# Kernel optimization log

Hardware: AMD Instinct MI355X
Metric: run time of the kernel (lower is better)

Reference implementation:

```python
import jax, jax.numpy as jnp
import numpy as np

B, Q, K, H = 8, 2048, 2048, 512


def setup_inputs() -> dict:
    key = jax.random.key(0)
    ks = jax.random.split(key, 12)
    s = 1.0 / np.sqrt(H)
    return {
        "query": jax.random.normal(ks[0], (B, Q, H), jnp.float32),
        "key_": jax.random.normal(ks[1], (B, K, H), jnp.float32),
        "value": jax.random.normal(ks[2], (B, K, H), jnp.float32),
        "mask": jax.random.randint(ks[3], (B, K), 0, 2).astype(bool),
        "Wq": jax.random.normal(ks[4], (H, H), jnp.float32) * s,
        "bq": jnp.zeros((H,), jnp.float32),
        "Wk": jax.random.normal(ks[5], (H, H), jnp.float32) * s,
        "bk": jnp.zeros((H,), jnp.float32),
        "Wv": jax.random.normal(ks[6], (H, H), jnp.float32) * s,
        "bv": jnp.zeros((H,), jnp.float32),
        "Wo": jax.random.normal(ks[7], (H, H), jnp.float32) * s,
        "bo": jnp.zeros((H,), jnp.float32),
    }


def reference(query, key_, value, mask, Wq, bq, Wk, bk, Wv, bv, Wo, bo):
    scale = jnp.sqrt(jnp.float32(H))
    Qp = query @ Wq + bq          # (B,Q,H)
    Kp = key_ @ Wk + bk           # (B,K,H)
    Vp = value @ Wv + bv          # (B,K,H)
    energy = jnp.einsum("bqh,bkh->bqk", Qp, Kp) / scale
    # mask is (B, key_len); torch code broadcasts it over all query rows
    energy = jnp.where(mask[:, None, :], -jnp.inf, energy)
    idx = jnp.argmax(energy, axis=-1)                 # (B,Q)
    score = jax.nn.one_hot(idx, K, dtype=energy.dtype)  # hardmax one-hot (B,Q,K)
    # score @ V is exactly a per-row gather of the argmax-selected V row
    res = jnp.take_along_axis(Vp, idx[:, :, None], axis=1)  # (B,Q,H)
    res = res @ Wo + bo
    return (res, score)
```

## Files before the change

kernel.cpp:

```cpp
#include <hip/hip_runtime.h>

typedef _Float16 f16;
typedef f16 f16x8 __attribute__((ext_vector_type(8)));
typedef f16 f16x4 __attribute__((ext_vector_type(4)));
typedef short s16x8 __attribute__((ext_vector_type(8)));
typedef short s16x4 __attribute__((ext_vector_type(4)));
typedef float f32x4 __attribute__((ext_vector_type(4)));

#define MFMA16(a,b,c)  __builtin_amdgcn_mfma_f32_16x16x32_f16(a,b,c,0,0,0)
#define MFMAB16(a,b,c) __builtin_amdgcn_mfma_f32_16x16x32_bf16(a,b,c,0,0,0)

static constexpr int Bn = 8, Qn = 2048, Kn = 2048, Hn = 512;
static constexpr int Mn = Bn * Qn;

typedef __attribute__((address_space(1))) const unsigned int as1_uint;
typedef __attribute__((address_space(3))) unsigned int as3_uint;

__device__ __forceinline__ void gl_lds16(const void* g, void* l) {
    __builtin_amdgcn_global_load_lds((as1_uint*)g, (as3_uint*)l, 16, 0, 0);
}

__device__ __forceinline__ short bf16r(float x) {
    unsigned u = __builtin_bit_cast(unsigned, x);
    u += 0x7fffu + ((u >> 16) & 1u);
    return (short)(u >> 16);
}

__device__ __forceinline__ int swz(int row) { return (row >> 1) & 3; }

__global__ __launch_bounds__(256) void compact_mask(
    const int* __restrict__ mask, int* __restrict__ cidx, int* __restrict__ cnt)
{
    __shared__ int sums[256];
    int b = blockIdx.x, t = threadIdx.x;
    int base = b * Kn + t * 8;
    int mv[8]; int s = 0;
    #pragma unroll
    for (int i = 0; i < 8; ++i) { mv[i] = (mask[base + i] == 0); s += mv[i]; }
    sums[t] = s;
    __syncthreads();
    for (int off = 1; off < 256; off <<= 1) {
        int v = (t >= off) ? sums[t - off] : 0;
        __syncthreads();
        sums[t] += v;
        __syncthreads();
    }
    int pos = (t > 0 ? sums[t - 1] : 0);
    #pragma unroll
    for (int i = 0; i < 8; ++i)
        if (mv[i]) cidx[b * Kn + pos++] = t * 8 + i;
    if (t == 255) {
        int total = sums[255];
        if (total == 0) { cidx[b * Kn] = 0; total = 1; }
        cnt[b] = total;
    }
}

__global__ __launch_bounds__(256) void prep_w(
    const float* __restrict__ Wq, const float* __restrict__ Wk,
    const float* __restrict__ Wv, const float* __restrict__ Wo,
    f16* __restrict__ Wqth, f16* __restrict__ Wqtl,
    f16* __restrict__ Wkth, f16* __restrict__ Wktl,
    short* __restrict__ Wvt, short* __restrict__ Wot)
{
    int e = blockIdx.x * 256 + threadIdx.x;
    int k = e >> 9, n = e & 511;
    int s = k * 512 + n, d = n * 512 + k;
    float wq = Wq[s] * 512.0f;
    f16 h = (f16)wq;
    Wqth[d] = h; Wqtl[d] = (f16)((wq - (float)h) * 2048.0f);
    float wk = Wk[s] * 512.0f;
    h = (f16)wk;
    Wkth[d] = h; Wktl[d] = (f16)((wk - (float)h) * 2048.0f);
    Wvt[d] = bf16r(Wv[s]);
    Wot[d] = bf16r(Wo[s]);
}

__global__ __launch_bounds__(256) void proj_fused(
    const float* __restrict__ query, const float* __restrict__ key_,
    const float* __restrict__ value,
    const f16* __restrict__ Wqth, const f16* __restrict__ Wqtl,
    const f16* __restrict__ Wkth, const f16* __restrict__ Wktl,
    const short* __restrict__ Wvt,
    const float* __restrict__ bq, const float* __restrict__ bk,
    const float* __restrict__ bvec,
    f16* __restrict__ Qp_h, f16* __restrict__ Qp_l,
    f16* __restrict__ Kc_h, f16* __restrict__ Kc_l,
    short* __restrict__ Vc,
    const int* __restrict__ cidx, const int* __restrict__ cnt)
{
    __shared__ __align__(16) char smem[49152];
    const int which = blockIdx.z;
    const int tid = threadIdx.x, lane = tid & 63, wid = tid >> 6;
    const int l15 = lane & 15, lg = lane >> 4;
    const int m0 = blockIdx.x * 64, n0 = blockIdx.y * 128;
    const int b = m0 >> 11, m0l = m0 & 2047;
    const int srow = lane >> 2, sg = lane & 3;
    const int ar0 = tid >> 3, ac0 = (tid & 7) * 4;

    int cn = 0;
    if (which > 0) {
        cn = cnt[b];
        if (m0l >= cn) return;
    }
    const float* Aptr = (which == 0) ? query : (which == 1 ? key_ : value);
    const float* aSrc[2];
    #pragma unroll
    for (int rr = 0; rr < 2; ++rr) {
        int row = ar0 + rr * 32;
        size_t grow;
        if (which > 0) {
            int r = m0l + row;
            int cid = (r < cn) ? cidx[b * Kn + r] : 0;
            grow = (size_t)(b * Kn + cid);
        } else {
            grow = (size_t)(m0 + row);
        }
        aSrc[rr] = Aptr + grow * Hn;
    }

    if (which < 2) {
        f16 (*Ah)[2048] = (f16(*)[2048])(smem);
        f16 (*Al)[2048] = (f16(*)[2048])(smem + 8192);
        f16 (*Bh)[4096] = (f16(*)[4096])(smem + 16384);
        f16 (*Bl)[4096] = (f16(*)[4096])(smem + 32768);
        const f16* Bth = (which == 0) ? Wqth : Wkth;
        const f16* Btl = (which == 0) ? Wqtl : Wktl;
        const float* bias = (which == 0) ? bq : bk;
        f16* Ph = (which == 0) ? Qp_h : Kc_h;
        f16* Pl = (which == 0) ? Qp_l : Kc_l;

        auto stageB = [&](int buf, int ks) {
            const int k0 = ks << 5;
            #pragma unroll
            for (int h = 0; h < 2; ++h) {
                int s = wid + h * 4;
                int row = s * 16 + srow;
                int goff = k0 + ((sg ^ swz(row)) << 3);
                gl_lds16(Bth + (size_t)(n0 + row) * Hn + goff, &Bh[buf][s * 512]);
                gl_lds16(Btl + (size_t)(n0 + row) * Hn + goff, &Bl[buf][s * 512]);
            }
        };
        auto writeA = [&](int buf, const f32x4* av) {
            #pragma unroll
            for (int rr = 0; rr < 2; ++rr) {
                int row = ar0 + rr * 32;
                f16x4 oh, ol;
                #pragma unroll
                for (int j = 0; j < 4; ++j) {
                    f16 hh = (f16)av[rr][j];
                    oh[j] = hh;
                    ol[j] = (f16)((av[rr][j] - (float)hh) * 2048.0f);
                }
                int off = row * 32 + (((ac0 >> 3) ^ swz(row)) << 3) + (ac0 & 7);
                *(f16x4*)&Ah[buf][off] = oh;
                *(f16x4*)&Al[buf][off] = ol;
            }
        };

        f32x4 a0[4][2] = {}, a1[4][2] = {};
        {
            f32x4 av[2];
            #pragma unroll
            for (int rr = 0; rr < 2; ++rr) av[rr] = *(const f32x4*)(aSrc[rr] + ac0);
            stageB(0, 0);
            writeA(0, av);
        }
        __syncthreads();
        #pragma unroll 1
        for (int ks = 0; ks < 16; ++ks) {
            const int cur = ks & 1, nxt = cur ^ 1;
            f32x4 av[2];
            if (ks < 15) {
                const int k1 = (ks + 1) << 5;
                #pragma unroll
                for (int rr = 0; rr < 2; ++rr) av[rr] = *(const f32x4*)(aSrc[rr] + k1 + ac0);
                stageB(nxt, ks + 1);
            }
            f16x8 fbh[2], fbl[2];
            #pragma unroll
            for (int fj = 0; fj < 2; ++fj) {
                int row = wid * 32 + fj * 16 + l15;
                int off = row * 32 + ((lg ^ swz(row)) << 3);
                fbh[fj] = *(f16x8*)&Bh[cur][off];
                fbl[fj] = *(f16x8*)&Bl[cur][off];
            }
            #pragma unroll
            for (int fi = 0; fi < 4; ++fi) {
                int row = fi * 16 + l15;
                int off = row * 32 + ((lg ^ swz(row)) << 3);
                f16x8 fah = *(f16x8*)&Ah[cur][off];
                f16x8 fal = *(f16x8*)&Al[cur][off];
                #pragma unroll
                for (int fj = 0; fj < 2; ++fj) {
                    a0[fi][fj] = MFMA16(fah, fbh[fj], a0[fi][fj]);
                    a1[fi][fj] = MFMA16(fah, fbl[fj], a1[fi][fj]);
                    a1[fi][fj] = MFMA16(fal, fbh[fj], a1[fi][fj]);
                }
            }
            if (ks < 15) writeA(nxt, av);
            __syncthreads();
        }
        #pragma unroll
        for (int fi = 0; fi < 4; ++fi)
        #pragma unroll
        for (int fj = 0; fj < 2; ++fj)
        #pragma unroll
        for (int j = 0; j < 4; ++j) {
            int m = m0 + fi * 16 + lg * 4 + j;
            int n = n0 + wid * 32 + fj * 16 + l15;
            float v = (a0[fi][fj][j] + a1[fi][fj][j] * (1.0f / 2048.0f)) * (1.0f / 512.0f) + bias[n];
            f16 h = (f16)v;
            Ph[(size_t)m * Hn + n] = h;
            Pl[(size_t)m * Hn + n] = (f16)((v - (float)h) * 2048.0f);
        }
    } else {
        short (*As)[2048] = (short(*)[2048])(smem);
        short (*Bs)[4096] = (short(*)[4096])(smem + 8192);

        auto stageB = [&](int buf, int ks) {
            const int k0 = ks << 5;
            #pragma unroll
            for (int h = 0; h < 2; ++h) {
                int s = wid + h * 4;
                int row = s * 16 + srow;
                int goff = k0 + ((sg ^ swz(row)) << 3);
                gl_lds16(Wvt + (size_t)(n0 + row) * Hn + goff, &Bs[buf][s * 512]);
            }
        };
        auto writeA = [&](int buf, const f32x4* av) {
            #pragma unroll
            for (int rr = 0; rr < 2; ++rr) {
                int row = ar0 + rr * 32;
                s16x4 o;
                #pragma unroll
                for (int j = 0; j < 4; ++j) o[j] = bf16r(av[rr][j]);
                int off = row * 32 + (((ac0 >> 3) ^ swz(row)) << 3) + (ac0 & 7);
                *(s16x4*)&As[buf][off] = o;
            }
        };

        f32x4 acc[4][2] = {};
        {
            f32x4 av[2];
            #pragma unroll
            for (int rr = 0; rr < 2; ++rr) av[rr] = *(const f32x4*)(aSrc[rr] + ac0);
            stageB(0, 0);
            writeA(0, av);
        }
        __syncthreads();
        #pragma unroll 1
        for (int ks = 0; ks < 16; ++ks) {
            const int cur = ks & 1, nxt = cur ^ 1;
            f32x4 av[2];
            if (ks < 15) {
                const int k1 = (ks + 1) << 5;
                #pragma unroll
                for (int rr = 0; rr < 2; ++rr) av[rr] = *(const f32x4*)(aSrc[rr] + k1 + ac0);
                stageB(nxt, ks + 1);
            }
            s16x8 fb[2];
            #pragma unroll
            for (int fj = 0; fj < 2; ++fj) {
                int row = wid * 32 + fj * 16 + l15;
                fb[fj] = *(s16x8*)&Bs[cur][row * 32 + ((lg ^ swz(row)) << 3)];
            }
            #pragma unroll
            for (int fi = 0; fi < 4; ++fi) {
                int row = fi * 16 + l15;
                s16x8 fa = *(s16x8*)&As[cur][row * 32 + ((lg ^ swz(row)) << 3)];
                #pragma unroll
                for (int fj = 0; fj < 2; ++fj)
                    acc[fi][fj] = MFMAB16(fa, fb[fj], acc[fi][fj]);
            }
            if (ks < 15) writeA(nxt, av);
            __syncthreads();
        }
        #pragma unroll
        for (int fi = 0; fi < 4; ++fi)
        #pragma unroll
        for (int fj = 0; fj < 2; ++fj)
        #pragma unroll
        for (int j = 0; j < 4; ++j) {
            int m = m0 + fi * 16 + lg * 4 + j;
            int n = n0 + wid * 32 + fj * 16 + l15;
            Vc[(size_t)m * Hn + n] = bf16r(acc[fi][fj][j] + bvec[n]);
        }
    }
}

__global__ __launch_bounds__(256) void energy_argmax(
    const f16* __restrict__ Qh, const f16* __restrict__ Ql,
    const f16* __restrict__ Kh, const f16* __restrict__ Kl,
    const int* __restrict__ cnt,
    float* __restrict__ pval, int* __restrict__ pidx)
{
    __shared__ __align__(16) f16 Ah[2][2048], Al[2][2048], Bh[2][4096], Bl[2][4096];
    __shared__ float bwv[4][64];
    __shared__ int   bwi[4][64];
    const int tid = threadIdx.x, lane = tid & 63, wid = tid >> 6;
    const int l15 = lane & 15, lg = lane >> 4;
    const int qt = blockIdx.x, kc = blockIdx.y, b = blockIdx.z;
    const int cn = cnt[b];
    const int kbase = kc << 7;
    if (kbase >= cn) return;
    const int m0 = b * Qn + qt * 64;
    const int kr0 = b * Kn + kbase;
    const float NEGINF = -__builtin_inff();
    const int srow = lane >> 2, sg = lane & 3;

    auto stage = [&](int buf, int ks) {
        const int k0 = ks << 5;
        {
            int row = wid * 16 + srow;
            int goff = k0 + ((sg ^ swz(row)) << 3);
            size_t ga = (size_t)(m0 + row) * Hn + goff;
            gl_lds16(Qh + ga, &Ah[buf][wid * 512]);
            gl_lds16(Ql + ga, &Al[buf][wid * 512]);
        }
        #pragma unroll
        for (int h = 0; h < 2; ++h) {
            int s = wid + h * 4;
            int row = s * 16 + srow;
            int goff = k0 + ((sg ^ swz(row)) << 3);
            size_t gb = (size_t)(kr0 + row) * Hn + goff;
            gl_lds16(Kh + gb, &Bh[buf][s * 512]);
            gl_lds16(Kl + gb, &Bl[buf][s * 512]);
        }
    };

    f32x4 a0[4][2] = {}, a1[4][2] = {};
    stage(0, 0);
    __syncthreads();
    #pragma unroll 1
    for (int ks = 0; ks < 16; ++ks) {
        const int cur = ks & 1;
        if (ks < 15) stage(cur ^ 1, ks + 1);
        f16x8 fbh[2], fbl[2];
        #pragma unroll
        for (int fj = 0; fj < 2; ++fj) {
            int row = wid * 32 + fj * 16 + l15;
            int off = row * 32 + ((lg ^ swz(row)) << 3);
            fbh[fj] = *(f16x8*)&Bh[cur][off];
            fbl[fj] = *(f16x8*)&Bl[cur][off];
        }
        #pragma unroll
        for (int fi = 0; fi < 4; ++fi) {
            int row = fi * 16 + l15;
            int off = row * 32 + ((lg ^ swz(row)) << 3);
            f16x8 fah = *(f16x8*)&Ah[cur][off];
            f16x8 fal = *(f16x8*)&Al[cur][off];
            #pragma unroll
            for (int fj = 0; fj < 2; ++fj) {
                a0[fi][fj] = MFMA16(fah, fbh[fj], a0[fi][fj]);
                a1[fi][fj] = MFMA16(fah, fbl[fj], a1[fi][fj]);
                a1[fi][fj] = MFMA16(fal, fbh[fj], a1[fi][fj]);
            }
        }
        __syncthreads();
    }
    #pragma unroll
    for (int fi = 0; fi < 4; ++fi) {
        #pragma unroll
        for (int j = 0; j < 4; ++j) {
            float bv = NEGINF; int bc = 0x7fffffff;
            #pragma unroll
            for (int fj = 0; fj < 2; ++fj) {
                int lc = wid * 32 + fj * 16 + l15;
                float v = a0[fi][fj][j] + a1[fi][fj][j] * (1.0f / 2048.0f);
                v = (kbase + lc < cn) ? v : NEGINF;
                if (v > bv || (v == bv && lc < bc)) { bv = v; bc = lc; }
            }
            #pragma unroll
            for (int sm = 1; sm < 16; sm <<= 1) {
                float ov = __shfl_xor(bv, sm, 64);
                int   oc = __shfl_xor(bc, sm, 64);
                if (ov > bv || (ov == bv && oc < bc)) { bv = ov; bc = oc; }
            }
            if (l15 == 0) {
                int row = fi * 16 + lg * 4 + j;
                bwv[wid][row] = bv; bwi[wid][row] = bc;
            }
        }
    }
    __syncthreads();
    if (tid < 64) {
        float bv = bwv[0][tid]; int bc = bwi[0][tid];
        #pragma unroll
        for (int s = 1; s < 4; ++s) {
            float v = bwv[s][tid]; int i = bwi[s][tid];
            if (v > bv || (v == bv && i < bc)) { bv = v; bc = i; }
        }
        int m = m0 + tid;
        pval[m * 16 + kc] = bv;
        pidx[m * 16 + kc] = kbase + bc;
    }
}

__global__ __launch_bounds__(256) void merge_gather(
    const float* __restrict__ pval, const int* __restrict__ pidx,
    const int* __restrict__ cnt, const int* __restrict__ cidx,
    const short* __restrict__ Vc, short* __restrict__ Vg, int* __restrict__ idxArr)
{
    int wid = threadIdx.x >> 6, lane = threadIdx.x & 63;
    int m = blockIdx.x * 4 + wid;
    int b = m >> 11;
    int nc = (cnt[b] + 127) >> 7;
    float bv = -__builtin_inff(); int bi = 0x7fffffff;
    for (int c = 0; c < nc; ++c) {
        float v = pval[m * 16 + c]; int i = pidx[m * 16 + c];
        if (v > bv || (v == bv && i < bi)) { bv = v; bi = i; }
    }
    if (lane == 0) idxArr[m] = cidx[b * Kn + bi];
    size_t src = ((size_t)(b * Kn + bi)) * Hn + lane * 8;
    size_t dst = (size_t)m * Hn + lane * 8;
    *(s16x8*)(Vg + dst) = *(const s16x8*)(Vc + src);
}

__global__ __launch_bounds__(256) void gemm_o(
    const short* __restrict__ A, const short* __restrict__ Bt,
    const float* __restrict__ bias, float* __restrict__ Out)
{
    __shared__ __align__(16) short As[2][4096], Bs[2][4096];
    const int tid = threadIdx.x, lane = tid & 63, wid = tid >> 6;
    const int wr = wid >> 1, wc = wid & 1, l15 = lane & 15, lg = lane >> 4;
    const int m0 = blockIdx.x * 128, n0 = blockIdx.y * 128;
    const int srow = lane >> 2, sg = lane & 3;
    f32x4 acc[4][4] = {};

    auto stage = [&](int buf, int ks) {
        const int k0 = ks << 5;
        #pragma unroll
        for (int h = 0; h < 2; ++h) {
            int s = wid + h * 4;
            int row = s * 16 + srow;
            int goff = k0 + ((sg ^ swz(row)) << 3);
            gl_lds16(A  + (size_t)(m0 + row) * Hn + goff, &As[buf][s * 512]);
            gl_lds16(Bt + (size_t)(n0 + row) * Hn + goff, &Bs[buf][s * 512]);
        }
    };

    stage(0, 0);
    __syncthreads();
    #pragma unroll 1
    for (int ks = 0; ks < 16; ++ks) {
        const int cur = ks & 1;
        if (ks < 15) stage(cur ^ 1, ks + 1);
        s16x8 fb[4];
        #pragma unroll
        for (int fj = 0; fj < 4; ++fj) {
            int row = wc * 64 + fj * 16 + l15;
            fb[fj] = *(s16x8*)&Bs[cur][row * 32 + ((lg ^ swz(row)) << 3)];
        }
        #pragma unroll
        for (int fi = 0; fi < 4; ++fi) {
            int row = wr * 64 + fi * 16 + l15;
            s16x8 fa = *(s16x8*)&As[cur][row * 32 + ((lg ^ swz(row)) << 3)];
            #pragma unroll
            for (int fj = 0; fj < 4; ++fj)
                acc[fi][fj] = MFMAB16(fa, fb[fj], acc[fi][fj]);
        }
        __syncthreads();
    }
    #pragma unroll
    for (int fi = 0; fi < 4; ++fi)
    #pragma unroll
    for (int fj = 0; fj < 4; ++fj)
    #pragma unroll
    for (int j = 0; j < 4; ++j) {
        int m = m0 + wr * 64 + fi * 16 + lg * 4 + j;
        int n = n0 + wc * 64 + fj * 16 + l15;
        Out[(size_t)m * Hn + n] = acc[fi][fj][j] + bias[n];
    }
}

__global__ __launch_bounds__(256) void score_fill(
    const int* __restrict__ idxArr, float* __restrict__ score)
{
    int m = blockIdx.x;
    int c = idxArr[m];
    float* row = score + (size_t)m * Kn;
    int t = threadIdx.x;
    #pragma unroll
    for (int i = 0; i < 2; ++i) {
        int v = t + i * 256;
        f32x4 val = {0.f, 0.f, 0.f, 0.f};
        if ((c >> 2) == v) val[c & 3] = 1.0f;
        *(f32x4*)(row + v * 4) = val;
    }
}

extern "C" void kernel_launch(void* const* d_in, const int* in_sizes, int n_in,
                              void* d_out, int out_size, void* d_ws, size_t ws_size,
                              hipStream_t stream)
{
    const float* query = (const float*)d_in[0];
    const float* key_  = (const float*)d_in[1];
    const float* value = (const float*)d_in[2];
    const int*   mask  = (const int*)d_in[3];
    const float* Wq = (const float*)d_in[4];
    const float* bq = (const float*)d_in[5];
    const float* Wk = (const float*)d_in[6];
    const float* bk = (const float*)d_in[7];
    const float* Wv = (const float*)d_in[8];
    const float* bv = (const float*)d_in[9];
    const float* Wo = (const float*)d_in[10];
    const float* bo = (const float*)d_in[11];

    float* res = (float*)d_out;
    float* scoreBase = res + (size_t)Mn * Hn;
    char* sc = (char*)scoreBase;
    const size_t MB16 = (size_t)Mn * Hn * 2;
    f16*   Qp_h = (f16*)(sc + 0 * MB16);
    f16*   Qp_l = (f16*)(sc + 1 * MB16);
    f16*   Kc_h = (f16*)(sc + 2 * MB16);
    f16*   Kc_l = (f16*)(sc + 3 * MB16);
    short* Vc   = (short*)(sc + 4 * MB16);
    char*  wb   = sc + 5 * MB16;
    f16*   Wqth = (f16*)(wb + 0 * 524288);
    f16*   Wqtl = (f16*)(wb + 1 * 524288);
    f16*   Wkth = (f16*)(wb + 2 * 524288);
    f16*   Wktl = (f16*)(wb + 3 * 524288);
    short* Wvt  = (short*)(wb + 4 * 524288);
    short* Wot  = (short*)(wb + 5 * 524288);
    int*   cidx = (int*)(wb + 6 * 524288);
    float* pval = (float*)(wb + 6 * 524288 + 65536);
    int*   pidx = (int*)(wb + 6 * 524288 + 65536 + 1048576);
    short* Vg   = (short*)(sc + 0 * MB16);

    int*   idxArr = (int*)d_ws;
    int*   cnt    = (int*)d_ws + Mn;

    compact_mask<<<Bn, 256, 0, stream>>>(mask, cidx, cnt);
    prep_w<<<1024, 256, 0, stream>>>(Wq, Wk, Wv, Wo, Wqth, Wqtl, Wkth, Wktl, Wvt, Wot);

    proj_fused<<<dim3(Mn / 64, Hn / 128, 3), 256, 0, stream>>>(
        query, key_, value, Wqth, Wqtl, Wkth, Wktl, Wvt,
        bq, bk, bv, Qp_h, Qp_l, Kc_h, Kc_l, Vc, cidx, cnt);

    energy_argmax<<<dim3(Qn / 64, 16, Bn), 256, 0, stream>>>(
        Qp_h, Qp_l, Kc_h, Kc_l, cnt, pval, pidx);

    merge_gather<<<Mn / 4, 256, 0, stream>>>(pval, pidx, cnt, cidx, Vc, Vg, idxArr);

    gemm_o<<<dim3(Mn / 128, Hn / 128), 256, 0, stream>>>(Vg, Wot, bo, res);

    score_fill<<<Mn, 256, 0, stream>>>(idxArr, scoreBase);
}
```

Measured before the change: 239.0 us.

## Fold weight products algebraically to skip K/V projections and gather raw inputs

Rewrites the pipeline using associativity. Wq·Wkᵀ and Wv·Wo are precomputed as small weight products, so the query is projected once through the combined matrix and the energy uses raw keys plus a per-key bias term. The V projection and the separate output GEMM become one GEMM on the gathered raw value rows. The score one-hot is now written with a memset followed by a scatter of ones instead of a full fill kernel. This removes the per-key K and V projection GEMMs and the intermediate V buffers, but adds small prep GEMMs and changes rounding behaviour, since the products are formed before splitting to f16/bf16.

```diff
diff --git a/kernel.cpp b/kernel.cpp
--- a/kernel.cpp
+++ b/kernel.cpp
@@ -56,243 +56,281 @@
     }
 }
 
-__global__ __launch_bounds__(256) void prep_w(
-    const float* __restrict__ Wq, const float* __restrict__ Wk,
-    const float* __restrict__ Wv, const float* __restrict__ Wo,
-    f16* __restrict__ Wqth, f16* __restrict__ Wqtl,
-    f16* __restrict__ Wkth, f16* __restrict__ Wktl,
-    short* __restrict__ Wvt, short* __restrict__ Wot)
+__global__ __launch_bounds__(256) void prep_split(
+    const float* __restrict__ Wk, const float* __restrict__ Wo,
+    f16* __restrict__ Wk_h, f16* __restrict__ Wk_l, short* __restrict__ Wot)
 {
     int e = blockIdx.x * 256 + threadIdx.x;
-    int k = e >> 9, n = e & 511;
-    int s = k * 512 + n, d = n * 512 + k;
-    float wq = Wq[s] * 512.0f;
-    f16 h = (f16)wq;
-    Wqth[d] = h; Wqtl[d] = (f16)((wq - (float)h) * 2048.0f);
-    float wk = Wk[s] * 512.0f;
-    h = (f16)wk;
-    Wkth[d] = h; Wktl[d] = (f16)((wk - (float)h) * 2048.0f);
-    Wvt[d] = bf16r(Wv[s]);
-    Wot[d] = bf16r(Wo[s]);
-}
-
-__global__ __launch_bounds__(256) void proj_fused(
-    const float* __restrict__ query, const float* __restrict__ key_,
-    const float* __restrict__ value,
-    const f16* __restrict__ Wqth, const f16* __restrict__ Wqtl,
-    const f16* __restrict__ Wkth, const f16* __restrict__ Wktl,
-    const short* __restrict__ Wvt,
-    const float* __restrict__ bq, const float* __restrict__ bk,
-    const float* __restrict__ bvec,
-    f16* __restrict__ Qp_h, f16* __restrict__ Qp_l,
-    f16* __restrict__ Kc_h, f16* __restrict__ Kc_l,
-    short* __restrict__ Vc,
-    const int* __restrict__ cidx, const int* __restrict__ cnt)
-{
-    __shared__ __align__(16) char smem[49152];
-    const int which = blockIdx.z;
+    float v = Wk[e] * 512.0f;
+    f16 h = (f16)v;
+    Wk_h[e] = h; Wk_l[e] = (f16)((v - (float)h) * 2048.0f);
+    int r = e >> 9, c = e & 511;
+    Wot[c * 512 + r] = bf16r(Wo[e]);
+}
+
+__global__ __launch_bounds__(512) void prep_vec(
+    const float* __restrict__ Wk, const float* __restrict__ Wo,
+    const float* __restrict__ bq, const float* __restrict__ bv,
+    const float* __restrict__ bo,
+    float* __restrict__ wvec, float* __restrict__ cvec)
+{
+    int t = threadIdx.x;
+    float s = 0.f;
+    for (int n = 0; n < 512; n += 4) {
+        f32x4 a = *(const f32x4*)(Wk + (size_t)t * 512 + n);
+        f32x4 q = *(const f32x4*)(bq + n);
+        s += a[0]*q[0] + a[1]*q[1] + a[2]*q[2] + a[3]*q[3];
+    }
+    wvec[t] = s;
+    float s2 = 0.f;
+    for (int h = 0; h < 512; ++h) s2 += bv[h] * Wo[h * 512 + t];
+    cvec[t] = s2 + bo[t];
+}
+
+template<int PREP>
+__global__ __launch_bounds__(256) void gemm_split(
+    const float* __restrict__ Af,
+    const f16* __restrict__ Bh_g, const f16* __restrict__ Bl_g,
+    f16* __restrict__ Oh, f16* __restrict__ Ol)
+{
+    __shared__ __align__(16) f16 Ah[2][2048], Al[2][2048], Bh[2][4096], Bl[2][4096];
     const int tid = threadIdx.x, lane = tid & 63, wid = tid >> 6;
     const int l15 = lane & 15, lg = lane >> 4;
     const int m0 = blockIdx.x * 64, n0 = blockIdx.y * 128;
-    const int b = m0 >> 11, m0l = m0 & 2047;
     const int srow = lane >> 2, sg = lane & 3;
     const int ar0 = tid >> 3, ac0 = (tid & 7) * 4;
 
-    int cn = 0;
-    if (which > 0) {
-        cn = cnt[b];
-        if (m0l >= cn) return;
-    }
-    const float* Aptr = (which == 0) ? query : (which == 1 ? key_ : value);
+    auto stageB = [&](int buf, int ks) {
+        const int k0 = ks << 5;
+        #pragma unroll
+        for (int h = 0; h < 2; ++h) {
+            int s = wid + h * 4;
+            int row = s * 16 + srow;
+            int goff = k0 + ((sg ^ swz(row)) << 3);
+            gl_lds16(Bh_g + (size_t)(n0 + row) * Hn + goff, &Bh[buf][s * 512]);
+            gl_lds16(Bl_g + (size_t)(n0 + row) * Hn + goff, &Bl[buf][s * 512]);
+        }
+    };
+    auto writeA = [&](int buf, const f32x4* av) {
+        #pragma unroll
+        for (int rr = 0; rr < 2; ++rr) {
+            int row = ar0 + rr * 32;
+            f16x4 oh, ol;
+            #pragma unroll
+            for (int j = 0; j < 4; ++j) {
+                f16 hh = (f16)av[rr][j];
+                oh[j] = hh;
+                ol[j] = (f16)((av[rr][j] - (float)hh) * 2048.0f);
+            }
+            int off = row * 32 + (((ac0 >> 3) ^ swz(row)) << 3) + (ac0 & 7);
+            *(f16x4*)&Ah[buf][off] = oh;
+            *(f16x4*)&Al[buf][off] = ol;
+        }
+    };
+
+    const float* aSrc[2];
+    #pragma unroll
+    for (int rr = 0; rr < 2; ++rr)
+        aSrc[rr] = Af + (size_t)(m0 + ar0 + rr * 32) * Hn;
+
+    f32x4 a0[4][2] = {}, a1[4][2] = {};
+    {
+        f32x4 av[2];
+        #pragma unroll
+        for (int rr = 0; rr < 2; ++rr) av[rr] = *(const f32x4*)(aSrc[rr] + ac0);
+        stageB(0, 0);
+        writeA(0, av);
+    }
+    __syncthreads();
+    #pragma unroll 1
+    for (int ks = 0; ks < 16; ++ks) {
+        const int cur = ks & 1, nxt = cur ^ 1;
+        f32x4 av[2];
+        if (ks < 15) {
+            const int k1 = (ks + 1) << 5;
+            #pragma unroll
+            for (int rr = 0; rr < 2; ++rr) av[rr] = *(const f32x4*)(aSrc[rr] + k1 + ac0);
+            stageB(nxt, ks + 1);
+        }
+        f16x8 fbh[2], fbl[2];
+        #pragma unroll
+        for (int fj = 0; fj < 2; ++fj) {
+            int row = wid * 32 + fj * 16 + l15;
+            int off = row * 32 + ((lg ^ swz(row)) << 3);
+            fbh[fj] = *(f16x8*)&Bh[cur][off];
+            fbl[fj] = *(f16x8*)&Bl[cur][off];
+        }
+        #pragma unroll
+        for (int fi = 0; fi < 4; ++fi) {
+            int row = fi * 16 + l15;
+            int off = row * 32 + ((lg ^ swz(row)) << 3);
+            f16x8 fah = *(f16x8*)&Ah[cur][off];
+            f16x8 fal = *(f16x8*)&Al[cur][off];
+            #pragma unroll
+            for (int fj = 0; fj < 2; ++fj) {
+                a0[fi][fj] = MFMA16(fah, fbh[fj], a0[fi][fj]);
+                a1[fi][fj] = MFMA16(fah, fbl[fj], a1[fi][fj]);
+                a1[fi][fj] = MFMA16(fal, fbh[fj], a1[fi][fj]);
+            }
+        }
+        if (ks < 15) writeA(nxt, av);
+        __syncthreads();
+    }
+    #pragma unroll
+    for (int fi = 0; fi < 4; ++fi)
+    #pragma unroll
+    for (int fj = 0; fj < 2; ++fj)
+    #pragma unroll
+    for (int j = 0; j < 4; ++j) {
+        int m = m0 + fi * 16 + lg * 4 + j;
+        int n = n0 + wid * 32 + fj * 16 + l15;
+        float v = a0[fi][fj][j] + a1[fi][fj][j] * (1.0f / 2048.0f);
+        if (PREP == 0) v *= (1.0f / 512.0f);
+        f16 h = (f16)v;
+        f16 lo = (f16)((v - (float)h) * 2048.0f);
+        size_t o = PREP ? ((size_t)n * Hn + m) : ((size_t)m * Hn + n);
+        Oh[o] = h; Ol[o] = lo;
+    }
+}
+
+template<int MODE>
+__global__ __launch_bounds__(256) void gemm_bfk(
+    const float* __restrict__ Af, const short* __restrict__ Bt,
+    const float* __restrict__ cvec, const int* __restrict__ idxArr,
+    void* __restrict__ Out)
+{
+    __shared__ __align__(16) short As[2][2048], Bs[2][4096];
+    const int tid = threadIdx.x, lane = tid & 63, wid = tid >> 6;
+    const int l15 = lane & 15, lg = lane >> 4;
+    const int m0 = blockIdx.x * 64, n0 = blockIdx.y * 128;
+    const int srow = lane >> 2, sg = lane & 3;
+    const int ar0 = tid >> 3, ac0 = (tid & 7) * 4;
+
     const float* aSrc[2];
     #pragma unroll
     for (int rr = 0; rr < 2; ++rr) {
         int row = ar0 + rr * 32;
         size_t grow;
-        if (which > 0) {
-            int r = m0l + row;
-            int cid = (r < cn) ? cidx[b * Kn + r] : 0;
-            grow = (size_t)(b * Kn + cid);
+        if (MODE == 1) {
+            int b = m0 >> 11;
+            grow = (size_t)(b * Kn + idxArr[m0 + row]);
         } else {
             grow = (size_t)(m0 + row);
         }
-        aSrc[rr] = Aptr + grow * Hn;
-    }
-
-    if (which < 2) {
-        f16 (*Ah)[2048] = (f16(*)[2048])(smem);
-        f16 (*Al)[2048] = (f16(*)[2048])(smem + 8192);
-        f16 (*Bh)[4096] = (f16(*)[4096])(smem + 16384);
-        f16 (*Bl)[4096] = (f16(*)[4096])(smem + 32768);
-        const f16* Bth = (which == 0) ? Wqth : Wkth;
-        const f16* Btl = (which == 0) ? Wqtl : Wktl;
-        const float* bias = (which == 0) ? bq : bk;
-        f16* Ph = (which == 0) ? Qp_h : Kc_h;
-        f16* Pl = (which == 0) ? Qp_l : Kc_l;
-
-        auto stageB = [&](int buf, int ks) {
-            const int k0 = ks << 5;
-            #pragma unroll
-            for (int h = 0; h < 2; ++h) {
-                int s = wid + h * 4;
-                int row = s * 16 + srow;
-                int goff = k0 + ((sg ^ swz(row)) << 3);
-                gl_lds16(Bth + (size_t)(n0 + row) * Hn + goff, &Bh[buf][s * 512]);
-                gl_lds16(Btl + (size_t)(n0 + row) * Hn + goff, &Bl[buf][s * 512]);
-            }
-        };
-        auto writeA = [&](int buf, const f32x4* av) {
-            #pragma unroll
-            for (int rr = 0; rr < 2; ++rr) {
-                int row = ar0 + rr * 32;
-                f16x4 oh, ol;
-                #pragma unroll
-                for (int j = 0; j < 4; ++j) {
-                    f16 hh = (f16)av[rr][j];
-                    oh[j] = hh;
-                    ol[j] = (f16)((av[rr][j] - (float)hh) * 2048.0f);
-                }
-                int off = row * 32 + (((ac0 >> 3) ^ swz(row)) << 3) + (ac0 & 7);
-                *(f16x4*)&Ah[buf][off] = oh;
-                *(f16x4*)&Al[buf][off] = ol;
-            }
-        };
-
-        f32x4 a0[4][2] = {}, a1[4][2] = {};
-        {
-            f32x4 av[2];
-            #pragma unroll
-            for (int rr = 0; rr < 2; ++rr) av[rr] = *(const f32x4*)(aSrc[rr] + ac0);
-            stageB(0, 0);
-            writeA(0, av);
-        }
+        aSrc[rr] = Af + grow * Hn;
+    }
+
+    auto stageB = [&](int buf, int ks) {
+        const int k0 = ks << 5;
+        #pragma unroll
+        for (int h = 0; h < 2; ++h) {
+            int s = wid + h * 4;
+            int row = s * 16 + srow;
+            int goff = k0 + ((sg ^ swz(row)) << 3);
+            gl_lds16(Bt + (size_t)(n0 + row) * Hn + goff, &Bs[buf][s * 512]);
+        }
+    };
+    auto writeA = [&](int buf, const f32x4* av) {
+        #pragma unroll
+        for (int rr = 0; rr < 2; ++rr) {
+            int row = ar0 + rr * 32;
+            s16x4 o;
+            #pragma unroll
+            for (int j = 0; j < 4; ++j) o[j] = bf16r(av[rr][j]);
+            int off = row * 32 + (((ac0 >> 3) ^ swz(row)) << 3) + (ac0 & 7);
+            *(s16x4*)&As[buf][off] = o;
+        }
+    };
+
+    f32x4 acc[4][2] = {};
+    {
+        f32x4 av[2];
+        #pragma unroll
+        for (int rr = 0; rr < 2; ++rr) av[rr] = *(const f32x4*)(aSrc[rr] + ac0);
+        stageB(0, 0);
+        writeA(0, av);
+    }
+    __syncthreads();
+    #pragma unroll 1
+    for (int ks = 0; ks < 16; ++ks) {
+        const int cur = ks & 1, nxt = cur ^ 1;
+        f32x4 av[2];
+        if (ks < 15) {
+            const int k1 = (ks + 1) << 5;
+            #pragma unroll
+            for (int rr = 0; rr < 2; ++rr) av[rr] = *(const f32x4*)(aSrc[rr] + k1 + ac0);
+            stageB(nxt, ks + 1);
+        }
+        s16x8 fb[2];
+        #pragma unroll
+        for (int fj = 0; fj < 2; ++fj) {
+            int row = wid * 32 + fj * 16 + l15;
+            fb[fj] = *(s16x8*)&Bs[cur][row * 32 + ((lg ^ swz(row)) << 3)];
+        }
+        #pragma unroll
+        for (int fi = 0; fi < 4; ++fi) {
+            int row = fi * 16 + l15;
+            s16x8 fa = *(s16x8*)&As[cur][row * 32 + ((lg ^ swz(row)) << 3)];
+            #pragma unroll
+            for (int fj = 0; fj < 2; ++fj)
+                acc[fi][fj] = MFMAB16(fa, fb[fj], acc[fi][fj]);
+        }
+        if (ks < 15) writeA(nxt, av);
         __syncthreads();
-        #pragma unroll 1
-        for (int ks = 0; ks < 16; ++ks) {
-            const int cur = ks & 1, nxt = cur ^ 1;
-            f32x4 av[2];
-            if (ks < 15) {
-                const int k1 = (ks + 1) << 5;
-                #pragma unroll
-                for (int rr = 0; rr < 2; ++rr) av[rr] = *(const f32x4*)(aSrc[rr] + k1 + ac0);
-                stageB(nxt, ks + 1);
-            }
-            f16x8 fbh[2], fbl[2];
-            #pragma unroll
-            for (int fj = 0; fj < 2; ++fj) {
-                int row = wid * 32 + fj * 16 + l15;
-                int off = row * 32 + ((lg ^ swz(row)) << 3);
-                fbh[fj] = *(f16x8*)&Bh[cur][off];
-                fbl[fj] = *(f16x8*)&Bl[cur][off];
-            }
-            #pragma unroll
-            for (int fi = 0; fi < 4; ++fi) {
-                int row = fi * 16 + l15;
-                int off = row * 32 + ((lg ^ swz(row)) << 3);
-                f16x8 fah = *(f16x8*)&Ah[cur][off];
-                f16x8 fal = *(f16x8*)&Al[cur][off];
-                #pragma unroll
-                for (int fj = 0; fj < 2; ++fj) {
-                    a0[fi][fj] = MFMA16(fah, fbh[fj], a0[fi][fj]);
-                    a1[fi][fj] = MFMA16(fah, fbl[fj], a1[fi][fj]);
-                    a1[fi][fj] = MFMA16(fal, fbh[fj], a1[fi][fj]);
-                }
-            }
-            if (ks < 15) writeA(nxt, av);
-            __syncthreads();
-        }
-        #pragma unroll
-        for (int fi = 0; fi < 4; ++fi)
-        #pragma unroll
-        for (int fj = 0; fj < 2; ++fj)
-        #pragma unroll
-        for (int j = 0; j < 4; ++j) {
-            int m = m0 + fi * 16 + lg * 4 + j;
-            int n = n0 + wid * 32 + fj * 16 + l15;
-            float v = (a0[fi][fj][j] + a1[fi][fj][j] * (1.0f / 2048.0f)) * (1.0f / 512.0f) + bias[n];
-            f16 h = (f16)v;
-            Ph[(size_t)m * Hn + n] = h;
-            Pl[(size_t)m * Hn + n] = (f16)((v - (float)h) * 2048.0f);
-        }
-    } else {
-        short (*As)[2048] = (short(*)[2048])(smem);
-        short (*Bs)[4096] = (short(*)[4096])(smem + 8192);
-
-        auto stageB = [&](int buf, int ks) {
-            const int k0 = ks << 5;
-            #pragma unroll
-            for (int h = 0; h < 2; ++h) {
-                int s = wid + h * 4;
-                int row = s * 16 + srow;
-                int goff = k0 + ((sg ^ swz(row)) << 3);
-                gl_lds16(Wvt + (size_t)(n0 + row) * Hn + goff, &Bs[buf][s * 512]);
-            }
-        };
-        auto writeA = [&](int buf, const f32x4* av) {
-            #pragma unroll
-            for (int rr = 0; rr < 2; ++rr) {
-                int row = ar0 + rr * 32;
-                s16x4 o;
-                #pragma unroll
-                for (int j = 0; j < 4; ++j) o[j] = bf16r(av[rr][j]);
-                int off = row * 32 + (((ac0 >> 3) ^ swz(row)) << 3) + (ac0 & 7);
-                *(s16x4*)&As[buf][off] = o;
-            }
-        };
-
-        f32x4 acc[4][2] = {};
-        {
-            f32x4 av[2];
-            #pragma unroll
-            for (int rr = 0; rr < 2; ++rr) av[rr] = *(const f32x4*)(aSrc[rr] + ac0);
-            stageB(0, 0);
-            writeA(0, av);
-        }
-        __syncthreads();
-        #pragma unroll 1
-        for (int ks = 0; ks < 16; ++ks) {
-            const int cur = ks & 1, nxt = cur ^ 1;
-            f32x4 av[2];
-            if (ks < 15) {
-                const int k1 = (ks + 1) << 5;
-                #pragma unroll
-                for (int rr = 0; rr < 2; ++rr) av[rr] = *(const f32x4*)(aSrc[rr] + k1 + ac0);
-                stageB(nxt, ks + 1);
-            }
-            s16x8 fb[2];
-            #pragma unroll
-            for (int fj = 0; fj < 2; ++fj) {
-                int row = wid * 32 + fj * 16 + l15;
-                fb[fj] = *(s16x8*)&Bs[cur][row * 32 + ((lg ^ swz(row)) << 3)];
-            }
-            #pragma unroll
-            for (int fi = 0; fi < 4; ++fi) {
-                int row = fi * 16 + l15;
-                s16x8 fa = *(s16x8*)&As[cur][row * 32 + ((lg ^ swz(row)) << 3)];
-                #pragma unroll
-                for (int fj = 0; fj < 2; ++fj)
-                    acc[fi][fj] = MFMAB16(fa, fb[fj], acc[fi][fj]);
-            }
-            if (ks < 15) writeA(nxt, av);
-            __syncthreads();
-        }
-        #pragma unroll
-        for (int fi = 0; fi < 4; ++fi)
-        #pragma unroll
-        for (int fj = 0; fj < 2; ++fj)
-        #pragma unroll
-        for (int j = 0; j < 4; ++j) {
-            int m = m0 + fi * 16 + lg * 4 + j;
-            int n = n0 + wid * 32 + fj * 16 + l15;
-            Vc[(size_t)m * Hn + n] = bf16r(acc[fi][fj][j] + bvec[n]);
-        }
-    }
+    }
+    #pragma unroll
+    for (int fi = 0; fi < 4; ++fi)
+    #pragma unroll
+    for (int fj = 0; fj < 2; ++fj)
+    #pragma unroll
+    for (int j = 0; j < 4; ++j) {
+        int m = m0 + fi * 16 + lg * 4 + j;
+        int n = n0 + wid * 32 + fj * 16 + l15;
+        if (MODE == 0) {
+            ((short*)Out)[(size_t)n * Hn + m] = bf16r(acc[fi][fj][j]);
+        } else {
+            ((float*)Out)[(size_t)m * Hn + n] = acc[fi][fj][j] + cvec[n];
+        }
+    }
+}
+
+__global__ __launch_bounds__(256) void kconv(
+    const float* __restrict__ key_, const int* __restrict__ cidx,
+    const int* __restrict__ cnt, const float* __restrict__ wvec,
+    f16* __restrict__ Kc_h, f16* __restrict__ Kc_l, float* __restrict__ beta)
+{
+    int wid = threadIdx.x >> 6, lane = threadIdx.x & 63;
+    int b = blockIdx.y, j = blockIdx.x * 4 + wid;
+    int cn = cnt[b];
+    if (j >= cn) return;
+    const float* src = key_ + (size_t)(b * Kn + cidx[b * Kn + j]) * Hn;
+    size_t dst = (size_t)(b * Kn + j) * Hn;
+    float s = 0.f;
+    #pragma unroll
+    for (int i = 0; i < 2; ++i) {
+        int c0 = lane * 8 + i * 4;
+        f32x4 v = *(const f32x4*)(src + c0);
+        f32x4 w = *(const f32x4*)(wvec + c0);
+        f16x4 oh, ol;
+        #pragma unroll
+        for (int e = 0; e < 4; ++e) {
+            f16 h = (f16)v[e];
+            oh[e] = h;
+            ol[e] = (f16)((v[e] - (float)h) * 2048.0f);
+            s += v[e] * w[e];
+        }
+        *(f16x4*)(Kc_h + dst + c0) = oh;
+        *(f16x4*)(Kc_l + dst + c0) = ol;
+    }
+    #pragma unroll
+    for (int sm = 1; sm < 64; sm <<= 1) s += __shfl_xor(s, sm, 64);
+    if (lane == 0) beta[b * Kn + j] = s;
 }
 
 __global__ __launch_bounds__(256) void energy_argmax(
     const f16* __restrict__ Qh, const f16* __restrict__ Ql,
     const f16* __restrict__ Kh, const f16* __restrict__ Kl,
-    const int* __restrict__ cnt,
+    const float* __restrict__ beta, const int* __restrict__ cnt,
     float* __restrict__ pval, int* __restrict__ pidx)
 {
     __shared__ __align__(16) f16 Ah[2][2048], Al[2][2048], Bh[2][4096], Bl[2][4096];
@@ -359,6 +397,12 @@
         }
         __syncthreads();
     }
+    float bet[2];
+    #pragma unroll
+    for (int fj = 0; fj < 2; ++fj) {
+        int lc = wid * 32 + fj * 16 + l15;
+        bet[fj] = beta[b * Kn + kbase + lc];
+    }
     #pragma unroll
     for (int fi = 0; fi < 4; ++fi) {
         #pragma unroll
@@ -367,7 +411,7 @@
             #pragma unroll
             for (int fj = 0; fj < 2; ++fj) {
                 int lc = wid * 32 + fj * 16 + l15;
-                float v = a0[fi][fj][j] + a1[fi][fj][j] * (1.0f / 2048.0f);
+                float v = a0[fi][fj][j] + a1[fi][fj][j] * (1.0f / 2048.0f) + bet[fj];
                 v = (kbase + lc < cn) ? v : NEGINF;
                 if (v > bv || (v == bv && lc < bc)) { bv = v; bc = lc; }
             }
@@ -397,13 +441,12 @@
     }
 }
 
-__global__ __launch_bounds__(256) void merge_gather(
+__global__ __launch_bounds__(256) void merge(
     const float* __restrict__ pval, const int* __restrict__ pidx,
     const int* __restrict__ cnt, const int* __restrict__ cidx,
-    const short* __restrict__ Vc, short* __restrict__ Vg, int* __restrict__ idxArr)
-{
-    int wid = threadIdx.x >> 6, lane = threadIdx.x & 63;
-    int m = blockIdx.x * 4 + wid;
+    int* __restrict__ idxArr)
+{
+    int m = blockIdx.x * 256 + threadIdx.x;
     int b = m >> 11;
     int nc = (cnt[b] + 127) >> 7;
     float bv = -__builtin_inff(); int bi = 0x7fffffff;
@@ -411,83 +454,14 @@
         float v = pval[m * 16 + c]; int i = pidx[m * 16 + c];
         if (v > bv || (v == bv && i < bi)) { bv = v; bi = i; }
     }
-    if (lane == 0) idxArr[m] = cidx[b * Kn + bi];
-    size_t src = ((size_t)(b * Kn + bi)) * Hn + lane * 8;
-    size_t dst = (size_t)m * Hn + lane * 8;
-    *(s16x8*)(Vg + dst) = *(const s16x8*)(Vc + src);
-}
-
-__global__ __launch_bounds__(256) void gemm_o(
-    const short* __restrict__ A, const short* __restrict__ Bt,
-    const float* __restrict__ bias, float* __restrict__ Out)
-{
-    __shared__ __align__(16) short As[2][4096], Bs[2][4096];
-    const int tid = threadIdx.x, lane = tid & 63, wid = tid >> 6;
-    const int wr = wid >> 1, wc = wid & 1, l15 = lane & 15, lg = lane >> 4;
-    const int m0 = blockIdx.x * 128, n0 = blockIdx.y * 128;
-    const int srow = lane >> 2, sg = lane & 3;
-    f32x4 acc[4][4] = {};
-
-    auto stage = [&](int buf, int ks) {
-        const int k0 = ks << 5;
-        #pragma unroll
-        for (int h = 0; h < 2; ++h) {
-            int s = wid + h * 4;
-            int row = s * 16 + srow;
-            int goff = k0 + ((sg ^ swz(row)) << 3);
-            gl_lds16(A  + (size_t)(m0 + row) * Hn + goff, &As[buf][s * 512]);
-            gl_lds16(Bt + (size_t)(n0 + row) * Hn + goff, &Bs[buf][s * 512]);
-        }
-    };
-
-    stage(0, 0);
-    __syncthreads();
-    #pragma unroll 1
-    for (int ks = 0; ks < 16; ++ks) {
-        const int cur = ks & 1;
-        if (ks < 15) stage(cur ^ 1, ks + 1);
-        s16x8 fb[4];
-        #pragma unroll
-        for (int fj = 0; fj < 4; ++fj) {
-            int row = wc * 64 + fj * 16 + l15;
-            fb[fj] = *(s16x8*)&Bs[cur][row * 32 + ((lg ^ swz(row)) << 3)];
-        }
-        #pragma unroll
-        for (int fi = 0; fi < 4; ++fi) {
-            int row = wr * 64 + fi * 16 + l15;
-            s16x8 fa = *(s16x8*)&As[cur][row * 32 + ((lg ^ swz(row)) << 3)];
-            #pragma unroll
-            for (int fj = 0; fj < 4; ++fj)
-                acc[fi][fj] = MFMAB16(fa, fb[fj], acc[fi][fj]);
-        }
-        __syncthreads();
-    }
-    #pragma unroll
-    for (int fi = 0; fi < 4; ++fi)
-    #pragma unroll
-    for (int fj = 0; fj < 4; ++fj)
-    #pragma unroll
-    for (int j = 0; j < 4; ++j) {
-        int m = m0 + wr * 64 + fi * 16 + lg * 4 + j;
-        int n = n0 + wc * 64 + fj * 16 + l15;
-        Out[(size_t)m * Hn + n] = acc[fi][fj][j] + bias[n];
-    }
-}
-
-__global__ __launch_bounds__(256) void score_fill(
+    idxArr[m] = cidx[b * Kn + bi];
+}
+
+__global__ __launch_bounds__(256) void scatter_ones(
     const int* __restrict__ idxArr, float* __restrict__ score)
 {
-    int m = blockIdx.x;
-    int c = idxArr[m];
-    float* row = score + (size_t)m * Kn;
-    int t = threadIdx.x;
-    #pragma unroll
-    for (int i = 0; i < 2; ++i) {
-        int v = t + i * 256;
-        f32x4 val = {0.f, 0.f, 0.f, 0.f};
-        if ((c >> 2) == v) val[c & 3] = 1.0f;
-        *(f32x4*)(row + v * 4) = val;
-    }
+    int m = blockIdx.x * 256 + threadIdx.x;
+    score[(size_t)m * Kn + idxArr[m]] = 1.0f;
 }
 
 extern "C" void kernel_launch(void* const* d_in, const int* in_sizes, int n_in,
@@ -501,49 +475,51 @@
     const float* Wq = (const float*)d_in[4];
     const float* bq = (const float*)d_in[5];
     const float* Wk = (const float*)d_in[6];
-    const float* bk = (const float*)d_in[7];
+    const float* bv = (const float*)d_in[9];
     const float* Wv = (const float*)d_in[8];
-    const float* bv = (const float*)d_in[9];
     const float* Wo = (const float*)d_in[10];
     const float* bo = (const float*)d_in[11];
 
     float* res = (float*)d_out;
     float* scoreBase = res + (size_t)Mn * Hn;
     char* sc = (char*)scoreBase;
-    const size_t MB16 = (size_t)Mn * Hn * 2;
-    f16*   Qp_h = (f16*)(sc + 0 * MB16);
-    f16*   Qp_l = (f16*)(sc + 1 * MB16);
-    f16*   Kc_h = (f16*)(sc + 2 * MB16);
-    f16*   Kc_l = (f16*)(sc + 3 * MB16);
-    short* Vc   = (short*)(sc + 4 * MB16);
-    char*  wb   = sc + 5 * MB16;
-    f16*   Wqth = (f16*)(wb + 0 * 524288);
-    f16*   Wqtl = (f16*)(wb + 1 * 524288);
-    f16*   Wkth = (f16*)(wb + 2 * 524288);
-    f16*   Wktl = (f16*)(wb + 3 * 524288);
-    short* Wvt  = (short*)(wb + 4 * 524288);
-    short* Wot  = (short*)(wb + 5 * 524288);
-    int*   cidx = (int*)(wb + 6 * 524288);
-    float* pval = (float*)(wb + 6 * 524288 + 65536);
-    int*   pidx = (int*)(wb + 6 * 524288 + 65536 + 1048576);
-    short* Vg   = (short*)(sc + 0 * MB16);
+    constexpr size_t MB = 1u << 20;
+    f16*   qM_h = (f16*)(sc + 0 * MB);
+    f16*   qM_l = (f16*)(sc + 16 * MB);
+    f16*   Kc_h = (f16*)(sc + 32 * MB);
+    f16*   Kc_l = (f16*)(sc + 48 * MB);
+    f16*   Mt_h = (f16*)(sc + 64 * MB);
+    f16*   Mt_l = (f16*)(sc + 64 * MB + 524288);
+    f16*   Wk_h = (f16*)(sc + 65 * MB);
+    f16*   Wk_l = (f16*)(sc + 65 * MB + 524288);
+    short* Wot  = (short*)(sc + 66 * MB);
+    short* NtB  = (short*)(sc + 66 * MB + 524288);
+    float* wvec = (float*)(sc + 67 * MB);
+    float* cvec = (float*)(sc + 67 * MB + 4096);
+    float* beta = (float*)(sc + 67 * MB + 8192);
+    float* pval = (float*)(sc + 67 * MB + 8192 + 65536);
+    int*   pidx = (int*)(sc + 68 * MB + 8192 + 65536);
+    int*   cidx = (int*)(sc + 69 * MB + 8192 + 65536);
 
     int*   idxArr = (int*)d_ws;
     int*   cnt    = (int*)d_ws + Mn;
 
     compact_mask<<<Bn, 256, 0, stream>>>(mask, cidx, cnt);
-    prep_w<<<1024, 256, 0, stream>>>(Wq, Wk, Wv, Wo, Wqth, Wqtl, Wkth, Wktl, Wvt, Wot);
-
-    proj_fused<<<dim3(Mn / 64, Hn / 128, 3), 256, 0, stream>>>(
-        query, key_, value, Wqth, Wqtl, Wkth, Wktl, Wvt,
-        bq, bk, bv, Qp_h, Qp_l, Kc_h, Kc_l, Vc, cidx, cnt);
+    prep_split<<<1024, 256, 0, stream>>>(Wk, Wo, Wk_h, Wk_l, Wot);
+    prep_vec<<<1, 512, 0, stream>>>(Wk, Wo, bq, bv, bo, wvec, cvec);
+
+    gemm_split<1><<<dim3(8, 4), 256, 0, stream>>>(Wq, Wk_h, Wk_l, Mt_h, Mt_l);
+    gemm_bfk<0><<<dim3(8, 4), 256, 0, stream>>>(Wv, Wot, nullptr, nullptr, NtB);
+    gemm_split<0><<<dim3(Mn / 64, 4), 256, 0, stream>>>(query, Mt_h, Mt_l, qM_h, qM_l);
+    kconv<<<dim3(512, Bn), 256, 0, stream>>>(key_, cidx, cnt, wvec, Kc_h, Kc_l, beta);
 
     energy_argmax<<<dim3(Qn / 64, 16, Bn), 256, 0, stream>>>(
-        Qp_h, Qp_l, Kc_h, Kc_l, cnt, pval, pidx);
-
-    merge_gather<<<Mn / 4, 256, 0, stream>>>(pval, pidx, cnt, cidx, Vc, Vg, idxArr);
-
-    gemm_o<<<dim3(Mn / 128, Hn / 128), 256, 0, stream>>>(Vg, Wot, bo, res);
-
-    score_fill<<<Mn, 256, 0, stream>>>(idxArr, scoreBase);
-}
+        qM_h, qM_l, Kc_h, Kc_l, beta, cnt, pval, pidx);
+
+    merge<<<Mn / 256, 256, 0, stream>>>(pval, pidx, cnt, cidx, idxArr);
+
+    gemm_bfk<1><<<dim3(Mn / 64, 4), 256, 0, stream>>>(value, NtB, cvec, idxArr, res);
+
+    hipMemsetAsync(scoreBase, 0, (size_t)Mn * Kn * 4, stream);
+    scatter_ones<<<Mn / 256, 256, 0, stream>>>(idxArr, scoreBase);
+}
```

After: 289.4 us. 1.21x slower.
